# Performance work log

Measured on AMD Instinct MI355X. Metric: run time of the kernel, lower is better.

## Reference

```python
import jax, jax.numpy as jnp
import numpy as np

N_NODES = 50000
N_EDGES = 600000
DIM = 128
VOCAB = 512
PAD_ID = 0
LN_EPS = 1e-5


def setup_inputs() -> dict:
    key = jax.random.key(0)
    ks = jax.random.split(key, 8)
    node_ids = jax.random.randint(ks[0], (N_NODES,), 0, VOCAB, dtype=jnp.int32)
    edge_index = jax.random.randint(ks[1], (2, N_EDGES), 0, N_NODES, dtype=jnp.int32)
    edge_weight = jax.random.uniform(ks[2], (N_EDGES,), dtype=jnp.float32)
    # embedding with padding row zeroed (padding_idx semantics)
    emb = jax.random.normal(ks[3], (VOCAB, DIM), dtype=jnp.float32) * 0.05
    emb = emb.at[PAD_ID].set(0.0)
    s = 1.0 / np.sqrt(DIM)
    W1 = jax.random.normal(ks[4], (DIM, DIM), dtype=jnp.float32) * s
    b1 = jnp.zeros((DIM,), jnp.float32)
    W2 = jax.random.normal(ks[5], (DIM, DIM), dtype=jnp.float32) * s
    b2 = jnp.zeros((DIM,), jnp.float32)
    return {
        "node_ids": node_ids, "edge_index": edge_index, "edge_weight": edge_weight,
        "emb": emb, "W1": W1, "b1": b1, "W2": W2, "b2": b2,
        "gamma1": jnp.ones((DIM,), jnp.float32), "beta1": jnp.zeros((DIM,), jnp.float32),
        "gamma2": jnp.ones((DIM,), jnp.float32), "beta2": jnp.zeros((DIM,), jnp.float32),
    }


def _gcn_conv(x, row, col, ew, W, b, n_nodes):
    """PyG GCNConv: normalize=True, add_self_loops=True, improved=False.
    Aggregation j->i: edge (row=src j, col=dst i)."""
    h = x @ W  # [N, out]
    # add self loops with weight 1
    loop = jnp.arange(n_nodes, dtype=row.dtype)
    row_f = jnp.concatenate([row, loop])
    col_f = jnp.concatenate([col, loop])
    ew_f = jnp.concatenate([ew, jnp.ones((n_nodes,), ew.dtype)])
    # symmetric degree normalization (deg over destination index)
    deg = jax.ops.segment_sum(ew_f, col_f, num_segments=n_nodes)
    dis = jnp.where(deg > 0, jax.lax.rsqrt(jnp.maximum(deg, 1e-12)), 0.0)
    norm = dis[row_f] * ew_f * dis[col_f]  # [E+N]
    msg = norm[:, None] * h[row_f]  # gather + scale  [E+N, out]
    out = jax.ops.segment_sum(msg, col_f, num_segments=n_nodes)  # scatter-add
    return out + b


def _layer_norm(x, gamma, beta):
    mu = jnp.mean(x, axis=-1, keepdims=True)
    var = jnp.mean(jnp.square(x - mu), axis=-1, keepdims=True)
    return (x - mu) * jax.lax.rsqrt(var + LN_EPS) * gamma + beta


def reference(node_ids, edge_index, edge_weight, emb, W1, b1, W2, b2,
              gamma1, beta1, gamma2, beta2):
    row, col = edge_index[0], edge_index[1]
    x = emb[node_ids]  # [N, D]
    x1 = _gcn_conv(x, row, col, edge_weight, W1, b1, N_NODES)
    x = _layer_norm(x + x1, gamma1, beta1)  # dropout is identity in eval
    x2 = _gcn_conv(x, row, col, edge_weight, W2, b2, N_NODES)
    x = _layer_norm(x + x2, gamma2, beta2)
    return x
```

## Files before the change

### kernel.cpp

```cpp
#include <hip/hip_runtime.h>

#define N_NODES 50000
#define N_EDGES 600000
#define DIM     128
#define VOCAB   512
#define LN_EPS  1e-5f
#define FIX20   1048576.0f
#define WSC     65535.0f
#define BCAP    64

typedef unsigned int uint;
typedef unsigned long long ull;
typedef unsigned short ushort;
typedef __attribute__((ext_vector_type(8))) short s8v;
typedef __attribute__((ext_vector_type(4))) float f4v;
typedef __attribute__((ext_vector_type(4))) int   i4v;
typedef __attribute__((ext_vector_type(4))) float fv4;
typedef __attribute__((ext_vector_type(2))) float f2v;

__device__ __forceinline__ uint f2bf(float f) {
    uint u = __float_as_uint(f);
    return (u + 0x7fffu + ((u >> 16) & 1u)) >> 16;
}
__device__ __forceinline__ float bf_lo(uint p) { return __uint_as_float(p << 16); }
__device__ __forceinline__ float bf_hi(uint p) { return __uint_as_float(p & 0xffff0000u); }
__device__ __forceinline__ float dis_of(uint pv) {
    return rsqrtf(1.0f + (float)(pv & 0x03ffffffu) * (1.0f / FIX20));
}

__global__ __launch_bounds__(256) void deg_mm1_kernel(
        const int* __restrict__ ei, const float* __restrict__ ew,
        uint2* pairN, const int* __restrict__ nid, uint* __restrict__ epack, int E,
        const float* __restrict__ X, const float* __restrict__ W,
        uint* __restrict__ Hb, int M,
        const float* __restrict__ W2, ushort* __restrict__ Wp) {
    __shared__ float Wt[32 * 128];
    __shared__ float Xt[64 * 36];
    int tid = threadIdx.x;
    int nbDeg = (E / 4 + 255) / 256;
    int nmm = (M + 63) / 64;
    if ((int)blockIdx.x < nbDeg) {
        int e0 = (blockIdx.x * 256 + tid) * 4;
        if (e0 >= E) return;
        i4v s4 = __builtin_nontemporal_load((const i4v*)(ei + e0));
        i4v c4 = __builtin_nontemporal_load((const i4v*)(ei + E + e0));
        fv4 w4 = __builtin_nontemporal_load((const fv4*)(ew + e0));
        int   s[4] = {s4.x, s4.y, s4.z, s4.w};
        int   c[4] = {c4.x, c4.y, c4.z, c4.w};
        float w[4] = {w4.x, w4.y, w4.z, w4.w};
        uint r[4];
        #pragma unroll
        for (int k = 0; k < 4; k++) {
            uint a = (1u << 26) | (uint)__float2int_rn(w[k] * FIX20);
            r[k] = atomicAdd(&((uint*)pairN)[2 * (size_t)c[k]], a);
        }
        #pragma unroll
        for (int k = 0; k < 4; k++) {
            uint rk = r[k] >> 26;
            uint wq = (uint)__float2int_rn(w[k] * WSC);
            epack[(size_t)c[k] * BCAP + rk] = (uint)s[k] | (wq << 16);
        }
        return;
    }
    if ((int)blockIdx.x >= nbDeg + nmm) {
        int o = (blockIdx.x - nbDeg - nmm) * 256 + tid;
        if (o < 16384) {
            int j = o & 7, lane = (o >> 3) & 63, chunk = o >> 9;
            int kc = chunk & 3, nc = chunk >> 2;
            int k = kc * 32 + (lane >> 4) * 8 + j;
            int n = nc * 16 + (lane & 15);
            Wp[o] = (ushort)f2bf(W2[k * 128 + n]);
        } else {
            int i = o - 16384;
            if (i < N_NODES) ((uint*)pairN)[2 * (size_t)i + 1] = (uint)nid[i];
        }
        return;
    }
    int bx = blockIdx.x - nbDeg;
    int tx = tid & 31, ty = tid >> 5;
    int r0 = bx * 64;
    float acc[8][4];
    #pragma unroll
    for (int j = 0; j < 8; j++)
        #pragma unroll
        for (int c = 0; c < 4; c++) acc[j][c] = 0.f;

    for (int kb = 0; kb < 128; kb += 32) {
        __syncthreads();
        #pragma unroll
        for (int q = 0; q < 4; q++) {
            int f = q * 256 + tid;
            ((float4*)Wt)[f] = *(const float4*)(W + kb * 128 + f * 4);
        }
        #pragma unroll
        for (int q = 0; q < 2; q++) {
            int f = q * 256 + tid;
            int row = f >> 3, cs = f & 7;
            int gr = r0 + row;
            float4 xv = make_float4(0.f, 0.f, 0.f, 0.f);
            if (gr < M) xv = *(const float4*)(X + (size_t)gr * 128 + kb + cs * 4);
            *(float4*)(Xt + row * 36 + cs * 4) = xv;
        }
        __syncthreads();
        #pragma unroll
        for (int k = 0; k < 32; k += 4) {
            float wv[4][4];
            #pragma unroll
            for (int kk = 0; kk < 4; kk++) {
                float4 t4 = *(const float4*)(Wt + (k + kk) * 128 + tx * 4);
                wv[kk][0] = t4.x; wv[kk][1] = t4.y; wv[kk][2] = t4.z; wv[kk][3] = t4.w;
            }
            #pragma unroll
            for (int j = 0; j < 8; j++) {
                float4 xv = *(const float4*)(Xt + (ty * 8 + j) * 36 + k);
                float xs[4] = {xv.x, xv.y, xv.z, xv.w};
                #pragma unroll
                for (int kk = 0; kk < 4; kk++)
                    #pragma unroll
                    for (int c = 0; c < 4; c++)
                        acc[j][c] = fmaf(xs[kk], wv[kk][c], acc[j][c]);
            }
        }
    }
    #pragma unroll
    for (int j = 0; j < 8; j++) {
        int gr = r0 + ty * 8 + j;
        if (gr < M) {
            uint p0 = f2bf(acc[j][0]) | (f2bf(acc[j][1]) << 16);
            uint p1 = f2bf(acc[j][2]) | (f2bf(acc[j][3]) << 16);
            ((uint2*)Hb)[(size_t)gr * 32 + tx] = make_uint2(p0, p1);
        }
    }
}

__global__ __launch_bounds__(256) void mm2_mfma(const uint* __restrict__ Xb,
                                                const ushort* __restrict__ Wp,
                                                const uint2* __restrict__ pairN,
                                                char* __restrict__ H8,
                                                float* __restrict__ rowscale, int M) {
    int wid = (blockIdx.x * 256 + threadIdx.x) >> 6;
    int lane = threadIdx.x & 63;
    int r0 = wid * 16;
    if (r0 >= M) return;
    int quad = lane >> 4, lo = lane & 15;
    const uint* xrow = Xb + (size_t)(r0 + lo) * 64 + quad * 4;
    s8v a[4];
    #pragma unroll
    for (int kc = 0; kc < 4; kc++) a[kc] = *(const s8v*)(xrow + kc * 16);
    f4v acc[8];
    #pragma unroll
    for (int nc = 0; nc < 8; nc++) {
        acc[nc] = (f4v){0.f, 0.f, 0.f, 0.f};
        #pragma unroll
        for (int kc = 0; kc < 4; kc++) {
            s8v b = *(const s8v*)(Wp + (size_t)((nc * 4 + kc) * 64 + lane) * 8);
            acc[nc] = __builtin_amdgcn_mfma_f32_16x16x32_bf16(a[kc], b, acc[nc], 0, 0, 0);
        }
    }
    float m[4];
    #pragma unroll
    for (int r = 0; r < 4; r++) {
        m[r] = 0.f;
        #pragma unroll
        for (int nc = 0; nc < 8; nc++) m[r] = fmaxf(m[r], fabsf(acc[nc][r]));
    }
    #pragma unroll
    for (int o = 1; o <= 8; o <<= 1)
        #pragma unroll
        for (int r = 0; r < 4; r++) m[r] = fmaxf(m[r], __shfl_xor(m[r], o, 64));
    #pragma unroll
    for (int r = 0; r < 4; r++) {
        float inv = (m[r] > 0.f) ? 127.0f / m[r] : 0.f;
        if (lo == 0) {
            int rr = r0 + quad * 4 + r;
            rowscale[rr] = m[r] * (1.0f / 127.0f) * dis_of(pairN[rr].x);
        }
        char* hp = H8 + (size_t)(r0 + quad * 4 + r) * 128 + lo;
        #pragma unroll
        for (int nc = 0; nc < 8; nc++)
            hp[nc * 16] = (char)__float2int_rn(acc[nc][r] * inv);
    }
}

template<bool RESID_BF, bool OUT_BF, bool GI8>
__global__ __launch_bounds__(256) void agg_ln(const uint2* __restrict__ pairN,
                                              const uint* __restrict__ epack,
                                              const void* __restrict__ hb,
                                              const float* __restrict__ rowscale,
                                              const void* __restrict__ resid,
                                              const float* __restrict__ bias,
                                              const float* __restrict__ gamma,
                                              const float* __restrict__ beta,
                                              void* __restrict__ out, int n) {
    int i = (blockIdx.x * 256 + threadIdx.x) >> 6;
    int lane = threadIdx.x & 63;
    if (i >= n) return;
    int iw = __builtin_amdgcn_readfirstlane(i);
    uint2 pnw = pairN[iw];
    uint pv = pnw.x;
    int deg = (int)(pv >> 26);
    float dl = dis_of(pv);
    int hri = GI8 ? iw : (int)pnw.y;
    float slo, shi;
    if (GI8) {
        uint ps = ((const ushort*)hb)[(size_t)hri * 64 + lane];
        float sc0 = rowscale[hri];
        slo = sc0 * (float)(signed char)(ps & 0xffu);
        shi = sc0 * (float)(signed char)(ps >> 8);
    } else {
        uint ps = ((const uint*)hb)[(size_t)hri * 64 + lane];
        slo = bf_lo(ps); shi = bf_hi(ps);
    }
    float sx[4] = {GI8 ? slo : dl * slo, 0.f, 0.f, 0.f};
    float sy[4] = {GI8 ? shi : dl * shi, 0.f, 0.f, 0.f};
    const uint* ep = epack + (size_t)iw * BCAP;

    for (int j0 = 0; j0 < deg; j0 += 16) {
        uint4 rv0 = ((const uint4*)(ep + j0))[0];
        uint4 rv1 = ((const uint4*)(ep + j0))[1];
        uint4 rv2 = ((const uint4*)(ep + j0))[2];
        uint4 rv3 = ((const uint4*)(ep + j0))[3];
        uint rec[16] = {rv0.x, rv0.y, rv0.z, rv0.w,
                        rv1.x, rv1.y, rv1.z, rv1.w,
                        rv2.x, rv2.y, rv2.z, rv2.w,
                        rv3.x, rv3.y, rv3.z, rv3.w};
        uint src[16];
        #pragma unroll
        for (int k = 0; k < 16; k++)
            src[k] = (j0 + k < deg) ? (rec[k] & 0xffffu) : 0u;
        uint qv[16];
        float scv[16];
        if (GI8) {
            #pragma unroll
            for (int k = 0; k < 16; k++)
                qv[k] = ((const ushort*)hb)[(size_t)src[k] * 64 + lane];
            #pragma unroll
            for (int k = 0; k < 16; k++)
                scv[k] = rowscale[src[k]];
        } else {
            uint2 pnk[16];
            #pragma unroll
            for (int k = 0; k < 16; k++)
                pnk[k] = pairN[src[k]];
            #pragma unroll
            for (int k = 0; k < 16; k++)
                qv[k] = ((const uint*)hb)[(size_t)pnk[k].y * 64 + lane];
            #pragma unroll
            for (int k = 0; k < 16; k++)
                scv[k] = (float)(pnk[k].x & 0x03ffffffu);
        }
        #pragma unroll
        for (int k = 0; k < 16; k++) {
            float w = (j0 + k < deg) ? (float)(rec[k] >> 16) * (1.0f / WSC) : 0.f;
            float lo, hi;
            if (GI8) {
                w *= scv[k];
                lo = (float)(signed char)(qv[k] & 0xffu);
                hi = (float)(signed char)(qv[k] >> 8);
            } else {
                w *= rsqrtf(1.0f + scv[k] * (1.0f / FIX20));
                lo = bf_lo(qv[k]); hi = bf_hi(qv[k]);
            }
            sx[k & 3] += w * lo;
            sy[k & 3] += w * hi;
        }
    }
    float acc0 = (sx[0] + sx[1]) + (sx[2] + sx[3]);
    float acc1 = (sy[0] + sy[1]) + (sy[2] + sy[3]);
    float2 xr;
    if (RESID_BF) {
        uint pr = __builtin_nontemporal_load((const uint*)resid + (size_t)hri * 64 + lane);
        xr = make_float2(bf_lo(pr), bf_hi(pr));
    } else {
        xr = ((const float2*)resid)[(size_t)hri * 64 + lane];
    }
    float2 bi = ((const float2*)bias)[lane];
    float v0 = xr.x + dl * acc0 + bi.x;
    float v1 = xr.y + dl * acc1 + bi.y;
    float s1 = v0 + v1, s2 = v0 * v0 + v1 * v1;
    #pragma unroll
    for (int o = 32; o > 0; o >>= 1) {
        s1 += __shfl_xor(s1, o, 64);
        s2 += __shfl_xor(s2, o, 64);
    }
    float mu   = s1 * (1.0f / DIM);
    float var  = s2 * (1.0f / DIM) - mu * mu;
    float rstd = rsqrtf(var + LN_EPS);
    float2 ga = ((const float2*)gamma)[lane];
    float2 be = ((const float2*)beta)[lane];
    float o0 = (v0 - mu) * rstd * ga.x + be.x;
    float o1 = (v1 - mu) * rstd * ga.y + be.y;
    if (OUT_BF) {
        __builtin_nontemporal_store(f2bf(o0) | (f2bf(o1) << 16),
                                    (uint*)out + (size_t)i * 64 + lane);
    } else {
        f2v ov = {o0, o1};
        __builtin_nontemporal_store(ov, (f2v*)((float2*)out + (size_t)i * 64 + lane));
    }
}

extern "C" void kernel_launch(void* const* d_in, const int* in_sizes, int n_in,
                              void* d_out, int out_size, void* d_ws, size_t ws_size,
                              hipStream_t stream) {
    const int*   node_ids = (const int*)  d_in[0];
    const int*   ei       = (const int*)  d_in[1];
    const float* ew       = (const float*)d_in[2];
    const float* emb      = (const float*)d_in[3];
    const float* W1       = (const float*)d_in[4];
    const float* b1       = (const float*)d_in[5];
    const float* W2       = (const float*)d_in[6];
    const float* b2       = (const float*)d_in[7];
    const float* g1       = (const float*)d_in[8];
    const float* be1      = (const float*)d_in[9];
    const float* g2       = (const float*)d_in[10];
    const float* be2      = (const float*)d_in[11];
    float* out = (float*)d_out;

    char* p = (char*)d_ws;
    auto alloc = [&](size_t bytes) {
        char* r = p;
        p += (bytes + 255) & ~(size_t)255;
        return r;
    };
    char*   h8      = (char*)  alloc((size_t)N_NODES * DIM);
    float*  rsc     = (float*) alloc((size_t)N_NODES * 4);
    uint*   x1b     = (uint*)  alloc((size_t)N_NODES * 64 * 4);
    uint*   hembB   = (uint*)  alloc((size_t)VOCAB * 64 * 4);
    ushort* Wp      = (ushort*)alloc((size_t)128 * 128 * 2);
    uint2*  pairN   = (uint2*) alloc((size_t)N_NODES * 8);
    uint*   epack   = (uint*)  alloc((size_t)N_NODES * BCAP * 4);

    int nbDeg = (N_EDGES / 4 + 255) / 256;
    int nmm = (VOCAB + 63) / 64;
    int nTail = 64 + (N_NODES + 255) / 256;

    (void)hipMemsetAsync(pairN, 0, (size_t)N_NODES * 8, stream);
    deg_mm1_kernel<<<nbDeg + nmm + nTail, 256, 0, stream>>>(
        ei, ew, pairN, node_ids, epack, N_EDGES, emb, W1, hembB, VOCAB, W2, Wp);

    agg_ln<false, true, false><<<(N_NODES + 3) / 4, 256, 0, stream>>>(
        pairN, epack, hembB, nullptr, emb, b1, g1, be1, x1b, N_NODES);

    mm2_mfma<<<(N_NODES / 16 + 3) / 4, 256, 0, stream>>>(x1b, Wp, pairN, h8, rsc, N_NODES);
    agg_ln<true, false, true><<<(N_NODES + 3) / 4, 256, 0, stream>>>(
        pairN, epack, h8, rsc, x1b, b2, g2, be2, out, N_NODES);
}
```

Measured before the change: 207.2 us.

## Fuse all GCN stages into one persistent kernel with grid barriers

Replaces the memset plus four separate kernel launches with a single persistent kernel of 512 blocks. Each stage runs in a grid-stride loop over virtual blocks, and stages are separated by an atomic-counter grid barrier. The aim is to remove launch gaps and kernel-boundary drains between the short stages. In exchange, parallelism is capped at 512 blocks with two blocks per CU, each stage waits on a spin barrier, and correctness depends on every block being co-resident.

```diff
diff --git a/kernel.cpp b/kernel.cpp
--- a/kernel.cpp
+++ b/kernel.cpp
@@ -8,6 +8,7 @@
 #define FIX20   1048576.0f
 #define WSC     65535.0f
 #define BCAP    64
+#define NBLK    512
 
 typedef unsigned int uint;
 typedef unsigned long long ull;
@@ -28,55 +29,65 @@
     return rsqrtf(1.0f + (float)(pv & 0x03ffffffu) * (1.0f / FIX20));
 }
 
-__global__ __launch_bounds__(256) void deg_mm1_kernel(
-        const int* __restrict__ ei, const float* __restrict__ ew,
-        uint2* pairN, const int* __restrict__ nid, uint* __restrict__ epack, int E,
-        const float* __restrict__ X, const float* __restrict__ W,
-        uint* __restrict__ Hb, int M,
-        const float* __restrict__ W2, ushort* __restrict__ Wp) {
-    __shared__ float Wt[32 * 128];
-    __shared__ float Xt[64 * 36];
-    int tid = threadIdx.x;
-    int nbDeg = (E / 4 + 255) / 256;
-    int nmm = (M + 63) / 64;
-    if ((int)blockIdx.x < nbDeg) {
-        int e0 = (blockIdx.x * 256 + tid) * 4;
-        if (e0 >= E) return;
-        i4v s4 = __builtin_nontemporal_load((const i4v*)(ei + e0));
-        i4v c4 = __builtin_nontemporal_load((const i4v*)(ei + E + e0));
-        fv4 w4 = __builtin_nontemporal_load((const fv4*)(ew + e0));
-        int   s[4] = {s4.x, s4.y, s4.z, s4.w};
-        int   c[4] = {c4.x, c4.y, c4.z, c4.w};
-        float w[4] = {w4.x, w4.y, w4.z, w4.w};
-        uint r[4];
-        #pragma unroll
-        for (int k = 0; k < 4; k++) {
-            uint a = (1u << 26) | (uint)__float2int_rn(w[k] * FIX20);
-            r[k] = atomicAdd(&((uint*)pairN)[2 * (size_t)c[k]], a);
-        }
-        #pragma unroll
-        for (int k = 0; k < 4; k++) {
-            uint rk = r[k] >> 26;
-            uint wq = (uint)__float2int_rn(w[k] * WSC);
-            epack[(size_t)c[k] * BCAP + rk] = (uint)s[k] | (wq << 16);
-        }
-        return;
-    }
-    if ((int)blockIdx.x >= nbDeg + nmm) {
-        int o = (blockIdx.x - nbDeg - nmm) * 256 + tid;
-        if (o < 16384) {
-            int j = o & 7, lane = (o >> 3) & 63, chunk = o >> 9;
-            int kc = chunk & 3, nc = chunk >> 2;
-            int k = kc * 32 + (lane >> 4) * 8 + j;
-            int n = nc * 16 + (lane & 15);
-            Wp[o] = (ushort)f2bf(W2[k * 128 + n]);
-        } else {
-            int i = o - 16384;
-            if (i < N_NODES) ((uint*)pairN)[2 * (size_t)i + 1] = (uint)nid[i];
-        }
-        return;
-    }
-    int bx = blockIdx.x - nbDeg;
+__device__ __forceinline__ void grid_bar(uint* cnt, uint target) {
+    __syncthreads();
+    __threadfence();
+    if (threadIdx.x == 0) {
+        __hip_atomic_fetch_add(cnt, 1u, __ATOMIC_RELEASE, __HIP_MEMORY_SCOPE_AGENT);
+        while (__hip_atomic_load(cnt, __ATOMIC_ACQUIRE, __HIP_MEMORY_SCOPE_AGENT)
+               < target)
+            __builtin_amdgcn_s_sleep(2);
+    }
+    __syncthreads();
+}
+
+struct GcnParams {
+    const int*   ei;
+    const float* ew;
+    uint2*       pairN;
+    const int*   nid;
+    uint*        epack;
+    const float* emb;
+    const float* W1;
+    uint*        hembB;
+    const float* W2;
+    ushort*      Wp;
+    uint*        x1b;
+    char*        h8;
+    float*       rsc;
+    const float* b1; const float* g1; const float* be1;
+    const float* b2; const float* g2; const float* be2;
+    float*       out;
+    uint*        bar;
+};
+
+__device__ __forceinline__ void deg_step(int vb, int tid, const GcnParams& P) {
+    int e0 = (vb * 256 + tid) * 4;
+    if (e0 >= N_EDGES) return;
+    i4v s4 = __builtin_nontemporal_load((const i4v*)(P.ei + e0));
+    i4v c4 = __builtin_nontemporal_load((const i4v*)(P.ei + N_EDGES + e0));
+    fv4 w4 = __builtin_nontemporal_load((const fv4*)(P.ew + e0));
+    int   s[4] = {s4.x, s4.y, s4.z, s4.w};
+    int   c[4] = {c4.x, c4.y, c4.z, c4.w};
+    float w[4] = {w4.x, w4.y, w4.z, w4.w};
+    uint r[4];
+    #pragma unroll
+    for (int k = 0; k < 4; k++) {
+        uint a = (1u << 26) | (uint)__float2int_rn(w[k] * FIX20);
+        r[k] = atomicAdd(&((uint*)P.pairN)[2 * (size_t)c[k]], a);
+    }
+    #pragma unroll
+    for (int k = 0; k < 4; k++) {
+        uint rk = r[k] >> 26;
+        uint wq = (uint)__float2int_rn(w[k] * WSC);
+        P.epack[(size_t)c[k] * BCAP + rk] = (uint)s[k] | (wq << 16);
+    }
+}
+
+__device__ __forceinline__ void mm1_step(int bx, int tid, float* Wt, float* Xt,
+                                         const GcnParams& P) {
+    const float* X = P.emb;
+    const float* W = P.W1;
     int tx = tid & 31, ty = tid >> 5;
     int r0 = bx * 64;
     float acc[8][4];
@@ -98,7 +109,7 @@
             int row = f >> 3, cs = f & 7;
             int gr = r0 + row;
             float4 xv = make_float4(0.f, 0.f, 0.f, 0.f);
-            if (gr < M) xv = *(const float4*)(X + (size_t)gr * 128 + kb + cs * 4);
+            if (gr < VOCAB) xv = *(const float4*)(X + (size_t)gr * 128 + kb + cs * 4);
             *(float4*)(Xt + row * 36 + cs * 4) = xv;
         }
         __syncthreads();
@@ -125,25 +136,32 @@
     #pragma unroll
     for (int j = 0; j < 8; j++) {
         int gr = r0 + ty * 8 + j;
-        if (gr < M) {
+        if (gr < VOCAB) {
             uint p0 = f2bf(acc[j][0]) | (f2bf(acc[j][1]) << 16);
             uint p1 = f2bf(acc[j][2]) | (f2bf(acc[j][3]) << 16);
-            ((uint2*)Hb)[(size_t)gr * 32 + tx] = make_uint2(p0, p1);
-        }
-    }
-}
-
-__global__ __launch_bounds__(256) void mm2_mfma(const uint* __restrict__ Xb,
-                                                const ushort* __restrict__ Wp,
-                                                const uint2* __restrict__ pairN,
-                                                char* __restrict__ H8,
-                                                float* __restrict__ rowscale, int M) {
-    int wid = (blockIdx.x * 256 + threadIdx.x) >> 6;
-    int lane = threadIdx.x & 63;
+            ((uint2*)P.hembB)[(size_t)gr * 32 + tx] = make_uint2(p0, p1);
+        }
+    }
+}
+
+__device__ __forceinline__ void prep_step(int o, const GcnParams& P) {
+    if (o < 16384) {
+        int j = o & 7, lane = (o >> 3) & 63, chunk = o >> 9;
+        int kc = chunk & 3, nc = chunk >> 2;
+        int k = kc * 32 + (lane >> 4) * 8 + j;
+        int n = nc * 16 + (lane & 15);
+        P.Wp[o] = (ushort)f2bf(P.W2[k * 128 + n]);
+    } else {
+        int i = o - 16384;
+        if (i < N_NODES) ((uint*)P.pairN)[2 * (size_t)i + 1] = (uint)P.nid[i];
+    }
+}
+
+__device__ __forceinline__ void mm2_step(int wid, int lane, const GcnParams& P) {
     int r0 = wid * 16;
-    if (r0 >= M) return;
+    if (r0 >= N_NODES) return;
     int quad = lane >> 4, lo = lane & 15;
-    const uint* xrow = Xb + (size_t)(r0 + lo) * 64 + quad * 4;
+    const uint* xrow = P.x1b + (size_t)(r0 + lo) * 64 + quad * 4;
     s8v a[4];
     #pragma unroll
     for (int kc = 0; kc < 4; kc++) a[kc] = *(const s8v*)(xrow + kc * 16);
@@ -153,7 +171,7 @@
         acc[nc] = (f4v){0.f, 0.f, 0.f, 0.f};
         #pragma unroll
         for (int kc = 0; kc < 4; kc++) {
-            s8v b = *(const s8v*)(Wp + (size_t)((nc * 4 + kc) * 64 + lane) * 8);
+            s8v b = *(const s8v*)(P.Wp + (size_t)((nc * 4 + kc) * 64 + lane) * 8);
             acc[nc] = __builtin_amdgcn_mfma_f32_16x16x32_bf16(a[kc], b, acc[nc], 0, 0, 0);
         }
     }
@@ -173,9 +191,9 @@
         float inv = (m[r] > 0.f) ? 127.0f / m[r] : 0.f;
         if (lo == 0) {
             int rr = r0 + quad * 4 + r;
-            rowscale[rr] = m[r] * (1.0f / 127.0f) * dis_of(pairN[rr].x);
-        }
-        char* hp = H8 + (size_t)(r0 + quad * 4 + r) * 128 + lo;
+            P.rsc[rr] = m[r] * (1.0f / 127.0f) * dis_of(P.pairN[rr].x);
+        }
+        char* hp = P.h8 + (size_t)(r0 + quad * 4 + r) * 128 + lo;
         #pragma unroll
         for (int nc = 0; nc < 8; nc++)
             hp[nc * 16] = (char)__float2int_rn(acc[nc][r] * inv);
@@ -183,18 +201,12 @@
 }
 
 template<bool RESID_BF, bool OUT_BF, bool GI8>
-__global__ __launch_bounds__(256) void agg_ln(const uint2* __restrict__ pairN,
-                                              const uint* __restrict__ epack,
-                                              const void* __restrict__ hb,
-                                              const float* __restrict__ rowscale,
-                                              const void* __restrict__ resid,
-                                              const float* __restrict__ bias,
-                                              const float* __restrict__ gamma,
-                                              const float* __restrict__ beta,
-                                              void* __restrict__ out, int n) {
-    int i = (blockIdx.x * 256 + threadIdx.x) >> 6;
-    int lane = threadIdx.x & 63;
-    if (i >= n) return;
+__device__ __forceinline__ void agg_step(int i, int lane,
+        const uint2* __restrict__ pairN, const uint* __restrict__ epack,
+        const void* __restrict__ hb, const float* __restrict__ rowscale,
+        const void* __restrict__ resid, const float* __restrict__ bias,
+        const float* __restrict__ gamma, const float* __restrict__ beta,
+        void* __restrict__ out) {
     int iw = __builtin_amdgcn_readfirstlane(i);
     uint2 pnw = pairN[iw];
     uint pv = pnw.x;
@@ -299,23 +311,54 @@
     }
 }
 
+__global__ __launch_bounds__(256, 2) void fused_gcn(GcnParams P) {
+    __shared__ float Wt[32 * 128];
+    __shared__ float Xt[64 * 36];
+    int tid = threadIdx.x;
+    int bid = blockIdx.x;
+    const int nb = NBLK;
+    int lane = tid & 63, wv = tid >> 6;
+
+    for (int t = bid * 256 + tid; t < N_NODES * 2; t += nb * 256)
+        ((uint*)P.pairN)[t] = 0u;
+    grid_bar(P.bar, 1 * nb);
+
+    constexpr int nbDeg = (N_EDGES / 4 + 255) / 256;
+    constexpr int nmm   = (VOCAB + 63) / 64;
+    constexpr int nTail = 64 + (N_NODES + 255) / 256;
+    constexpr int NVB1  = nbDeg + nmm + nTail;
+    for (int vb = bid; vb < NVB1; vb += nb) {
+        if (vb < nbDeg)            deg_step(vb, tid, P);
+        else if (vb < nbDeg + nmm) mm1_step(vb - nbDeg, tid, Wt, Xt, P);
+        else                       prep_step((vb - nbDeg - nmm) * 256 + tid, P);
+    }
+    grid_bar(P.bar, 2 * nb);
+
+    constexpr int NVBA = (N_NODES + 3) / 4;
+    for (int vb = bid; vb < NVBA; vb += nb) {
+        int i = vb * 4 + wv;
+        if (i < N_NODES)
+            agg_step<false, true, false>(i, lane, P.pairN, P.epack, P.hembB,
+                                         nullptr, P.emb, P.b1, P.g1, P.be1, P.x1b);
+    }
+    grid_bar(P.bar, 3 * nb);
+
+    constexpr int NVB3 = (N_NODES / 16 + 3) / 4;
+    for (int vb = bid; vb < NVB3; vb += nb)
+        mm2_step(vb * 4 + wv, lane, P);
+    grid_bar(P.bar, 4 * nb);
+
+    for (int vb = bid; vb < NVBA; vb += nb) {
+        int i = vb * 4 + wv;
+        if (i < N_NODES)
+            agg_step<true, false, true>(i, lane, P.pairN, P.epack, P.h8,
+                                        P.rsc, P.x1b, P.b2, P.g2, P.be2, P.out);
+    }
+}
+
 extern "C" void kernel_launch(void* const* d_in, const int* in_sizes, int n_in,
                               void* d_out, int out_size, void* d_ws, size_t ws_size,
                               hipStream_t stream) {
-    const int*   node_ids = (const int*)  d_in[0];
-    const int*   ei       = (const int*)  d_in[1];
-    const float* ew       = (const float*)d_in[2];
-    const float* emb      = (const float*)d_in[3];
-    const float* W1       = (const float*)d_in[4];
-    const float* b1       = (const float*)d_in[5];
-    const float* W2       = (const float*)d_in[6];
-    const float* b2       = (const float*)d_in[7];
-    const float* g1       = (const float*)d_in[8];
-    const float* be1      = (const float*)d_in[9];
-    const float* g2       = (const float*)d_in[10];
-    const float* be2      = (const float*)d_in[11];
-    float* out = (float*)d_out;
-
     char* p = (char*)d_ws;
     auto alloc = [&](size_t bytes) {
         char* r = p;
@@ -329,19 +372,31 @@
     ushort* Wp      = (ushort*)alloc((size_t)128 * 128 * 2);
     uint2*  pairN   = (uint2*) alloc((size_t)N_NODES * 8);
     uint*   epack   = (uint*)  alloc((size_t)N_NODES * BCAP * 4);
-
-    int nbDeg = (N_EDGES / 4 + 255) / 256;
-    int nmm = (VOCAB + 63) / 64;
-    int nTail = 64 + (N_NODES + 255) / 256;
-
-    (void)hipMemsetAsync(pairN, 0, (size_t)N_NODES * 8, stream);
-    deg_mm1_kernel<<<nbDeg + nmm + nTail, 256, 0, stream>>>(
-        ei, ew, pairN, node_ids, epack, N_EDGES, emb, W1, hembB, VOCAB, W2, Wp);
-
-    agg_ln<false, true, false><<<(N_NODES + 3) / 4, 256, 0, stream>>>(
-        pairN, epack, hembB, nullptr, emb, b1, g1, be1, x1b, N_NODES);
-
-    mm2_mfma<<<(N_NODES / 16 + 3) / 4, 256, 0, stream>>>(x1b, Wp, pairN, h8, rsc, N_NODES);
-    agg_ln<true, false, true><<<(N_NODES + 3) / 4, 256, 0, stream>>>(
-        pairN, epack, h8, rsc, x1b, b2, g2, be2, out, N_NODES);
-}
+    uint*   bar     = (uint*)  alloc(256);
+
+    GcnParams P;
+    P.ei    = (const int*)  d_in[1];
+    P.ew    = (const float*)d_in[2];
+    P.pairN = pairN;
+    P.nid   = (const int*)  d_in[0];
+    P.epack = epack;
+    P.emb   = (const float*)d_in[3];
+    P.W1    = (const float*)d_in[4];
+    P.hembB = hembB;
+    P.W2    = (const float*)d_in[6];
+    P.Wp    = Wp;
+    P.x1b   = x1b;
+    P.h8    = h8;
+    P.rsc   = rsc;
+    P.b1    = (const float*)d_in[5];
+    P.g1    = (const float*)d_in[8];
+    P.be1   = (const float*)d_in[9];
+    P.b2    = (const float*)d_in[7];
+    P.g2    = (const float*)d_in[10];
+    P.be2   = (const float*)d_in[11];
+    P.out   = (float*)d_out;
+    P.bar   = bar;
+
+    (void)hipMemsetAsync(bar, 0, 256, stream);
+    fused_gcn<<<NBLK, 256, 0, stream>>>(P);
+}
```

New measurement: 701.4 us. 238% more time.

## Fuse layer-1 aggregation+LayerNorm with layer-2 MFMA matmul in one kernel

Applied to the files above, without the earlier changes.

Merges the first aggregation/LayerNorm kernel with the second-layer bf16 MFMA matmul and int8 quantization. Each 256-thread block aggregates 16 nodes (4 per wave), stages the bf16 rows in LDS, and each wave computes two 16-column output chunks. Per-row max is reduced across waves through shared memory. This removes one launch and the global reread of x1b for the matmul. The cost is lower per-wave matmul work, extra block syncs, and serialized aggregation before the MFMA phase.

```diff
diff --git a/kernel.cpp b/kernel.cpp
--- a/kernel.cpp
+++ b/kernel.cpp
@@ -133,86 +133,21 @@
     }
 }
 
-__global__ __launch_bounds__(256) void mm2_mfma(const uint* __restrict__ Xb,
-                                                const ushort* __restrict__ Wp,
-                                                const uint2* __restrict__ pairN,
-                                                char* __restrict__ H8,
-                                                float* __restrict__ rowscale, int M) {
-    int wid = (blockIdx.x * 256 + threadIdx.x) >> 6;
-    int lane = threadIdx.x & 63;
-    int r0 = wid * 16;
-    if (r0 >= M) return;
-    int quad = lane >> 4, lo = lane & 15;
-    const uint* xrow = Xb + (size_t)(r0 + lo) * 64 + quad * 4;
-    s8v a[4];
-    #pragma unroll
-    for (int kc = 0; kc < 4; kc++) a[kc] = *(const s8v*)(xrow + kc * 16);
-    f4v acc[8];
-    #pragma unroll
-    for (int nc = 0; nc < 8; nc++) {
-        acc[nc] = (f4v){0.f, 0.f, 0.f, 0.f};
-        #pragma unroll
-        for (int kc = 0; kc < 4; kc++) {
-            s8v b = *(const s8v*)(Wp + (size_t)((nc * 4 + kc) * 64 + lane) * 8);
-            acc[nc] = __builtin_amdgcn_mfma_f32_16x16x32_bf16(a[kc], b, acc[nc], 0, 0, 0);
-        }
-    }
-    float m[4];
-    #pragma unroll
-    for (int r = 0; r < 4; r++) {
-        m[r] = 0.f;
-        #pragma unroll
-        for (int nc = 0; nc < 8; nc++) m[r] = fmaxf(m[r], fabsf(acc[nc][r]));
-    }
-    #pragma unroll
-    for (int o = 1; o <= 8; o <<= 1)
-        #pragma unroll
-        for (int r = 0; r < 4; r++) m[r] = fmaxf(m[r], __shfl_xor(m[r], o, 64));
-    #pragma unroll
-    for (int r = 0; r < 4; r++) {
-        float inv = (m[r] > 0.f) ? 127.0f / m[r] : 0.f;
-        if (lo == 0) {
-            int rr = r0 + quad * 4 + r;
-            rowscale[rr] = m[r] * (1.0f / 127.0f) * dis_of(pairN[rr].x);
-        }
-        char* hp = H8 + (size_t)(r0 + quad * 4 + r) * 128 + lo;
-        #pragma unroll
-        for (int nc = 0; nc < 8; nc++)
-            hp[nc * 16] = (char)__float2int_rn(acc[nc][r] * inv);
-    }
-}
-
-template<bool RESID_BF, bool OUT_BF, bool GI8>
-__global__ __launch_bounds__(256) void agg_ln(const uint2* __restrict__ pairN,
-                                              const uint* __restrict__ epack,
-                                              const void* __restrict__ hb,
-                                              const float* __restrict__ rowscale,
-                                              const void* __restrict__ resid,
-                                              const float* __restrict__ bias,
-                                              const float* __restrict__ gamma,
-                                              const float* __restrict__ beta,
-                                              void* __restrict__ out, int n) {
-    int i = (blockIdx.x * 256 + threadIdx.x) >> 6;
-    int lane = threadIdx.x & 63;
-    if (i >= n) return;
+__device__ __forceinline__ uint agg1_node(int i, int lane,
+        const uint2* __restrict__ pairN, const uint* __restrict__ epack,
+        const uint* __restrict__ hb, const float* __restrict__ emb,
+        const float* __restrict__ bias, const float* __restrict__ gamma,
+        const float* __restrict__ beta, uint* __restrict__ x1b) {
     int iw = __builtin_amdgcn_readfirstlane(i);
     uint2 pnw = pairN[iw];
     uint pv = pnw.x;
     int deg = (int)(pv >> 26);
     float dl = dis_of(pv);
-    int hri = GI8 ? iw : (int)pnw.y;
-    float slo, shi;
-    if (GI8) {
-        uint ps = ((const ushort*)hb)[(size_t)hri * 64 + lane];
-        float sc0 = rowscale[hri];
-        slo = sc0 * (float)(signed char)(ps & 0xffu);
-        shi = sc0 * (float)(signed char)(ps >> 8);
-    } else {
-        uint ps = ((const uint*)hb)[(size_t)hri * 64 + lane];
-        slo = bf_lo(ps); shi = bf_hi(ps);
-    }
-    float sx[4] = {GI8 ? slo : dl * slo, 0.f, 0.f, 0.f};
-    float sy[4] = {GI8 ? shi : dl * shi, 0.f, 0.f, 0.f};
+    int hri = (int)pnw.y;
+    uint ps = hb[(size_t)hri * 64 + lane];
+    float slo = bf_lo(ps), shi = bf_hi(ps);
+    float sx[4] = {dl * slo, 0.f, 0.f, 0.f};
+    float sy[4] = {dl * shi, 0.f, 0.f, 0.f};
     const uint* ep = epack + (size_t)iw * BCAP;
 
     for (int j0 = 0; j0 < deg; j0 += 16) {
@@ -228,52 +163,25 @@
         #pragma unroll
         for (int k = 0; k < 16; k++)
             src[k] = (j0 + k < deg) ? (rec[k] & 0xffffu) : 0u;
+        uint2 pnk[16];
+        #pragma unroll
+        for (int k = 0; k < 16; k++)
+            pnk[k] = pairN[src[k]];
         uint qv[16];
-        float scv[16];
-        if (GI8) {
-            #pragma unroll
-            for (int k = 0; k < 16; k++)
-                qv[k] = ((const ushort*)hb)[(size_t)src[k] * 64 + lane];
-            #pragma unroll
-            for (int k = 0; k < 16; k++)
-                scv[k] = rowscale[src[k]];
-        } else {
-            uint2 pnk[16];
-            #pragma unroll
-            for (int k = 0; k < 16; k++)
-                pnk[k] = pairN[src[k]];
-            #pragma unroll
-            for (int k = 0; k < 16; k++)
-                qv[k] = ((const uint*)hb)[(size_t)pnk[k].y * 64 + lane];
-            #pragma unroll
-            for (int k = 0; k < 16; k++)
-                scv[k] = (float)(pnk[k].x & 0x03ffffffu);
-        }
+        #pragma unroll
+        for (int k = 0; k < 16; k++)
+            qv[k] = hb[(size_t)pnk[k].y * 64 + lane];
         #pragma unroll
         for (int k = 0; k < 16; k++) {
             float w = (j0 + k < deg) ? (float)(rec[k] >> 16) * (1.0f / WSC) : 0.f;
-            float lo, hi;
-            if (GI8) {
-                w *= scv[k];
-                lo = (float)(signed char)(qv[k] & 0xffu);
-                hi = (float)(signed char)(qv[k] >> 8);
-            } else {
-                w *= rsqrtf(1.0f + scv[k] * (1.0f / FIX20));
-                lo = bf_lo(qv[k]); hi = bf_hi(qv[k]);
-            }
-            sx[k & 3] += w * lo;
-            sy[k & 3] += w * hi;
+            w *= rsqrtf(1.0f + (float)(pnk[k].x & 0x03ffffffu) * (1.0f / FIX20));
+            sx[k & 3] += w * bf_lo(qv[k]);
+            sy[k & 3] += w * bf_hi(qv[k]);
         }
     }
     float acc0 = (sx[0] + sx[1]) + (sx[2] + sx[3]);
     float acc1 = (sy[0] + sy[1]) + (sy[2] + sy[3]);
-    float2 xr;
-    if (RESID_BF) {
-        uint pr = __builtin_nontemporal_load((const uint*)resid + (size_t)hri * 64 + lane);
-        xr = make_float2(bf_lo(pr), bf_hi(pr));
-    } else {
-        xr = ((const float2*)resid)[(size_t)hri * 64 + lane];
-    }
+    float2 xr = ((const float2*)emb)[(size_t)hri * 64 + lane];
     float2 bi = ((const float2*)bias)[lane];
     float v0 = xr.x + dl * acc0 + bi.x;
     float v1 = xr.y + dl * acc1 + bi.y;
@@ -290,13 +198,157 @@
     float2 be = ((const float2*)beta)[lane];
     float o0 = (v0 - mu) * rstd * ga.x + be.x;
     float o1 = (v1 - mu) * rstd * ga.y + be.y;
-    if (OUT_BF) {
-        __builtin_nontemporal_store(f2bf(o0) | (f2bf(o1) << 16),
-                                    (uint*)out + (size_t)i * 64 + lane);
-    } else {
-        f2v ov = {o0, o1};
-        __builtin_nontemporal_store(ov, (f2v*)((float2*)out + (size_t)i * 64 + lane));
-    }
+    uint pw = f2bf(o0) | (f2bf(o1) << 16);
+    __builtin_nontemporal_store(pw, x1b + (size_t)i * 64 + lane);
+    return pw;
+}
+
+__global__ __launch_bounds__(256) void agg1_mm2(
+        const uint2* __restrict__ pairN, const uint* __restrict__ epack,
+        const uint* __restrict__ hembB, const ushort* __restrict__ Wp,
+        const float* __restrict__ emb,
+        const float* __restrict__ b1, const float* __restrict__ g1,
+        const float* __restrict__ be1,
+        uint* __restrict__ x1b, char* __restrict__ h8,
+        float* __restrict__ rsc) {
+    __shared__ uint  Xs[16][68];
+    __shared__ float wmax[4][4][4];
+    int tid = threadIdx.x, lane = tid & 63, wv = tid >> 6;
+    int b0 = blockIdx.x * 16;
+
+    #pragma unroll
+    for (int t = 0; t < 4; t++) {
+        int row = wv * 4 + t;
+        uint pw = agg1_node(b0 + row, lane, pairN, epack, hembB, emb,
+                            b1, g1, be1, x1b);
+        Xs[row][lane] = pw;
+    }
+    __syncthreads();
+
+    int quad = lane >> 4, lo = lane & 15;
+    s8v a[4];
+    #pragma unroll
+    for (int kc = 0; kc < 4; kc++)
+        a[kc] = *(const s8v*)&Xs[lo][quad * 4 + kc * 16];
+    f4v acc[2];
+    #pragma unroll
+    for (int c = 0; c < 2; c++) {
+        int nc = wv * 2 + c;
+        acc[c] = (f4v){0.f, 0.f, 0.f, 0.f};
+        #pragma unroll
+        for (int kc = 0; kc < 4; kc++) {
+            s8v b = *(const s8v*)(Wp + (size_t)((nc * 4 + kc) * 64 + lane) * 8);
+            acc[c] = __builtin_amdgcn_mfma_f32_16x16x32_bf16(a[kc], b, acc[c], 0, 0, 0);
+        }
+    }
+    float m[4];
+    #pragma unroll
+    for (int r = 0; r < 4; r++)
+        m[r] = fmaxf(fabsf(acc[0][r]), fabsf(acc[1][r]));
+    #pragma unroll
+    for (int o = 1; o <= 8; o <<= 1)
+        #pragma unroll
+        for (int r = 0; r < 4; r++) m[r] = fmaxf(m[r], __shfl_xor(m[r], o, 64));
+    if (lo == 0)
+        #pragma unroll
+        for (int r = 0; r < 4; r++) wmax[wv][quad][r] = m[r];
+    __syncthreads();
+    float fm[4];
+    #pragma unroll
+    for (int r = 0; r < 4; r++)
+        fm[r] = fmaxf(fmaxf(wmax[0][quad][r], wmax[1][quad][r]),
+                      fmaxf(wmax[2][quad][r], wmax[3][quad][r]));
+    #pragma unroll
+    for (int r = 0; r < 4; r++) {
+        float inv = (fm[r] > 0.f) ? 127.0f / fm[r] : 0.f;
+        char* hp = h8 + (size_t)(b0 + quad * 4 + r) * 128 + lo;
+        #pragma unroll
+        for (int c = 0; c < 2; c++)
+            hp[(wv * 2 + c) * 16] = (char)__float2int_rn(acc[c][r] * inv);
+    }
+    if (wv == 0 && lo == 0) {
+        #pragma unroll
+        for (int r = 0; r < 4; r++) {
+            int rr = b0 + quad * 4 + r;
+            rsc[rr] = fm[r] * (1.0f / 127.0f) * dis_of(pairN[rr].x);
+        }
+    }
+}
+
+__global__ __launch_bounds__(256) void agg2_ln(const uint2* __restrict__ pairN,
+                                               const uint* __restrict__ epack,
+                                               const ushort* __restrict__ hb,
+                                               const float* __restrict__ rowscale,
+                                               const uint* __restrict__ resid,
+                                               const float* __restrict__ bias,
+                                               const float* __restrict__ gamma,
+                                               const float* __restrict__ beta,
+                                               float* __restrict__ out, int n) {
+    int i = (blockIdx.x * 256 + threadIdx.x) >> 6;
+    int lane = threadIdx.x & 63;
+    if (i >= n) return;
+    int iw = __builtin_amdgcn_readfirstlane(i);
+    uint pv = pairN[iw].x;
+    int deg = (int)(pv >> 26);
+    float dl = dis_of(pv);
+    uint ps = hb[(size_t)iw * 64 + lane];
+    float sc0 = rowscale[iw];
+    float slo = sc0 * (float)(signed char)(ps & 0xffu);
+    float shi = sc0 * (float)(signed char)(ps >> 8);
+    float sx[4] = {slo, 0.f, 0.f, 0.f};
+    float sy[4] = {shi, 0.f, 0.f, 0.f};
+    const uint* ep = epack + (size_t)iw * BCAP;
+
+    for (int j0 = 0; j0 < deg; j0 += 16) {
+        uint4 rv0 = ((const uint4*)(ep + j0))[0];
+        uint4 rv1 = ((const uint4*)(ep + j0))[1];
+        uint4 rv2 = ((const uint4*)(ep + j0))[2];
+        uint4 rv3 = ((const uint4*)(ep + j0))[3];
+        uint rec[16] = {rv0.x, rv0.y, rv0.z, rv0.w,
+                        rv1.x, rv1.y, rv1.z, rv1.w,
+                        rv2.x, rv2.y, rv2.z, rv2.w,
+                        rv3.x, rv3.y, rv3.z, rv3.w};
+        uint src[16];
+        #pragma unroll
+        for (int k = 0; k < 16; k++)
+            src[k] = (j0 + k < deg) ? (rec[k] & 0xffffu) : 0u;
+        uint qv[16];
+        float scv[16];
+        #pragma unroll
+        for (int k = 0; k < 16; k++)
+            qv[k] = hb[(size_t)src[k] * 64 + lane];
+        #pragma unroll
+        for (int k = 0; k < 16; k++)
+            scv[k] = rowscale[src[k]];
+        #pragma unroll
+        for (int k = 0; k < 16; k++) {
+            float w = (j0 + k < deg) ? (float)(rec[k] >> 16) * (1.0f / WSC) : 0.f;
+            w *= scv[k];
+            sx[k & 3] += w * (float)(signed char)(qv[k] & 0xffu);
+            sy[k & 3] += w * (float)(signed char)(qv[k] >> 8);
+        }
+    }
+    float acc0 = (sx[0] + sx[1]) + (sx[2] + sx[3]);
+    float acc1 = (sy[0] + sy[1]) + (sy[2] + sy[3]);
+    uint pr = __builtin_nontemporal_load(resid + (size_t)iw * 64 + lane);
+    float2 bi = ((const float2*)bias)[lane];
+    float v0 = bf_lo(pr) + dl * acc0 + bi.x;
+    float v1 = bf_hi(pr) + dl * acc1 + bi.y;
+    float s1 = v0 + v1, s2 = v0 * v0 + v1 * v1;
+    #pragma unroll
+    for (int o = 32; o > 0; o >>= 1) {
+        s1 += __shfl_xor(s1, o, 64);
+        s2 += __shfl_xor(s2, o, 64);
+    }
+    float mu   = s1 * (1.0f / DIM);
+    float var  = s2 * (1.0f / DIM) - mu * mu;
+    float rstd = rsqrtf(var + LN_EPS);
+    float2 ga = ((const float2*)gamma)[lane];
+    float2 be = ((const float2*)beta)[lane];
+    float o0 = (v0 - mu) * rstd * ga.x + be.x;
+    float o1 = (v1 - mu) * rstd * ga.y + be.y;
+    f2v ov = {o0, o1};
+    __builtin_nontemporal_store(ov, (f2v*)((float2*)out + (size_t)i * 64 + lane));
 }
 
 extern "C" void kernel_launch(void* const* d_in, const int* in_sizes, int n_in,
@@ -338,10 +390,9 @@
     deg_mm1_kernel<<<nbDeg + nmm + nTail, 256, 0, stream>>>(
         ei, ew, pairN, node_ids, epack, N_EDGES, emb, W1, hembB, VOCAB, W2, Wp);
 
-    agg_ln<false, true, false><<<(N_NODES + 3) / 4, 256, 0, stream>>>(
-        pairN, epack, hembB, nullptr, emb, b1, g1, be1, x1b, N_NODES);
-
-    mm2_mfma<<<(N_NODES / 16 + 3) / 4, 256, 0, stream>>>(x1b, Wp, pairN, h8, rsc, N_NODES);
-    agg_ln<true, false, true><<<(N_NODES + 3) / 4, 256, 0, stream>>>(
-        pairN, epack, h8, rsc, x1b, b2, g2, be2, out, N_NODES);
-}
+    agg1_mm2<<<N_NODES / 16, 256, 0, stream>>>(
+        pairN, epack, hembB, Wp, emb, b1, g1, be1, x1b, h8, rsc);
+
+    agg2_ln<<<(N_NODES + 3) / 4, 256, 0, stream>>>(
+        pairN, epack, (const ushort*)h8, rsc, x1b, b2, g2, be2, out, N_NODES);
+}
```

New measurement: 207.7 us. About the same (+0.2%).
